# Optimization experiments

Measured on AMD Instinct MI355X. Metric: run time of the kernel, lower is better.

Reference implementation:

```python
import jax, jax.numpy as jnp
import numpy as np

B, T, C, H = 2, 2048, 1024, 16
HS = C // H  # head size = 64


def _rope_cos_sin(t, hs):
    # theta_i = 1/10000^(2(i-1)/hs) for i in [1, hs/2]
    pos = jnp.arange(t, dtype=jnp.float32)[:, None]          # [T,1]
    i = jnp.arange(1, hs // 2 + 1, dtype=jnp.float32)[None]  # [1,hs/2]
    theta = 1.0 / 10000.0 ** (2.0 * (i - 1.0) / hs)
    ang = pos * theta                                        # [T,hs/2]
    return jnp.cos(ang), jnp.sin(ang)


def _apply_rope(u, cos, sin):
    # u: [B,H,T,HS]; complex multiply on consecutive pairs
    u2 = u.reshape(*u.shape[:-1], HS // 2, 2)
    x0, x1 = u2[..., 0], u2[..., 1]
    c = cos[None, None]  # [1,1,T,hs/2]
    s = sin[None, None]
    r0 = x0 * c - x1 * s
    r1 = x0 * s + x1 * c
    return jnp.stack([r0, r1], axis=-1).reshape(u.shape)


def setup_inputs() -> dict:
    key = jax.random.key(0)
    ks = jax.random.split(key, 5)
    return {
        "x": jax.random.normal(ks[0], (B, T, C), dtype=jnp.float32),
        "W_qkv": jax.random.normal(ks[1], (C, 3 * C), dtype=jnp.float32) * 0.02,
        "b_qkv": jax.random.normal(ks[2], (3 * C,), dtype=jnp.float32) * 0.02,
        "W_proj": jax.random.normal(ks[3], (C, C), dtype=jnp.float32) * 0.02,
        "b_proj": jax.random.normal(ks[4], (C,), dtype=jnp.float32) * 0.02,
    }


def reference(x, W_qkv, b_qkv, W_proj, b_proj):
    b, t, c = x.shape
    qkv = x @ W_qkv + b_qkv                                   # [B,T,3C]
    qkv = qkv.reshape(b, t, H, 3 * HS).transpose(0, 2, 1, 3)  # [B,H,T,3*HS]
    q, k, v = jnp.split(qkv, 3, axis=-1)                      # each [B,H,T,HS]

    cos, sin = _rope_cos_sin(t, HS)
    q = _apply_rope(q, cos, sin)
    k = _apply_rope(k, cos, sin)

    att = jnp.einsum("bhqd,bhkd->bhqk", q, k) / jnp.sqrt(jnp.float32(HS))
    causal = jnp.tril(jnp.ones((t, t), dtype=bool))[None, None]
    att = jnp.where(causal, att, jnp.float32(-1e9))
    att = jax.nn.softmax(att, axis=-1)
    y = jnp.einsum("bhqk,bhkd->bhqd", att, v)                 # [B,H,T,HS]
    y = y.transpose(0, 2, 1, 3).reshape(b, t, c)
    return y @ W_proj + b_proj
```

## Files before the change

### kernel.cpp

```cpp
#include <hip/hip_runtime.h>

typedef unsigned short u16;
typedef unsigned int u32;
typedef __bf16 bf16x8 __attribute__((ext_vector_type(8)));
typedef float f32x4 __attribute__((ext_vector_type(4)));
typedef float f32x16 __attribute__((ext_vector_type(16)));
typedef u32 u32x4 __attribute__((ext_vector_type(4)));
typedef u16 u16x4 __attribute__((ext_vector_type(4)));
typedef u16 u16x8 __attribute__((ext_vector_type(8)));

__device__ __forceinline__ u16 f2bf(float f) {
  u32 u = __builtin_bit_cast(u32, f);
  u += 0x7fffu + ((u >> 16) & 1u);
  return (u16)(u >> 16);
}

__device__ __forceinline__ u32 pk2(float a, float b) {
  u32 ua = __builtin_bit_cast(u32, a) + 0x8000u;
  u32 ub = __builtin_bit_cast(u32, b) + 0x8000u;
  return __builtin_amdgcn_perm(ub, ua, 0x07060302);
}

__device__ __forceinline__ u32 cpk(float a, float b) {
  u32 r;
  asm("v_cvt_pk_bf16_f32 %0, %1, %2" : "=v"(r) : "v"(a), "v"(b));
  return r;
}

__device__ __forceinline__ void gld16(const void* g, void* l) {
  __builtin_amdgcn_global_load_lds(
      (const __attribute__((address_space(1))) void*)g,
      (__attribute__((address_space(3))) void*)l, 16, 0, 0);
}

__global__ __launch_bounds__(256) void k_prep(
    const float* __restrict__ x, u16* __restrict__ xb,
    const float* __restrict__ Wqkv, u16* __restrict__ Wqkvt,
    const float* __restrict__ Wproj, u16* __restrict__ Wpt,
    float2* __restrict__ rope) {
  __shared__ float tile[32][33];
  const int tid = threadIdx.x;
  int bx = blockIdx.x;
  if (bx < 4096) {
    int i = (bx * 256 + tid) * 4;
    float4 v = *(const float4*)(x + i);
    u16x4 o = { f2bf(v.x), f2bf(v.y), f2bf(v.z), f2bf(v.w) };
    *(u16x4*)(xb + i) = o;
    return;
  }
  bx -= 4096;
  const float* src; u16* dst; int R, Cc, bxx, byy;
  if (bx < 3072) {
    src = Wqkv; dst = Wqkvt; R = 1024; Cc = 3072; bxx = bx % 96; byy = bx / 96;
  } else if (bx < 4096) {
    int b = bx - 3072;
    src = Wproj; dst = Wpt; R = 1024; Cc = 1024; bxx = b % 32; byy = b / 32;
  } else {
    int i = (bx - 4096) * 256 + tid;
    int t = i >> 5, d = i & 31;
    float theta = expf(-(float)d * 0.28782313662425575f);
    float ang = (float)t * theta;
    rope[i] = make_float2(cosf(ang), sinf(ang));
    return;
  }
  int xx = tid & 31, yy = tid >> 5;
  int c0 = bxx * 32, r0 = byy * 32;
  for (int i = 0; i < 4; ++i)
    tile[yy + 8 * i][xx] = src[(size_t)(r0 + yy + 8 * i) * Cc + c0 + xx];
  __syncthreads();
  for (int i = 0; i < 4; ++i)
    dst[(size_t)(c0 + yy + 8 * i) * R + r0 + xx] = f2bf(tile[xx][yy + 8 * i]);
}

__global__ __launch_bounds__(256, 4) void k_qkv(
    const u16* __restrict__ Xb,
    const u16* __restrict__ Wt,
    const float* __restrict__ bias,
    const float2* __restrict__ rope,
    u16* __restrict__ Qg,
    u16* __restrict__ Kg,
    u16* __restrict__ Vt) {
  __shared__ alignas(16) u16 smem[18432];
  u16* As = smem;
  u16* Bs = smem + 8192;
  const int tid = threadIdx.x;
  const int lane = tid & 63, w = tid >> 6;
  const int quad = lane >> 4, l15 = lane & 15;
  const int m0 = blockIdx.y * 128, n0 = blockIdx.x * 128;
  const int wm = (w & 1) * 64, wn = (w >> 1) * 64;
  const int srow = lane >> 3, sj = lane & 7;
  const int sw = (sj ^ srow) * 8;
  const f32x4 vzero = {0.f, 0.f, 0.f, 0.f};

  f32x4 acc[4][4];
  for (int i = 0; i < 4; ++i)
    for (int j = 0; j < 4; ++j) acc[i][j] = vzero;

  for (int kt = 0; kt < 1024; kt += 64) {
    __syncthreads();
    for (int i = 0; i < 4; ++i) {
      int row = w * 32 + i * 8;
      gld16(Xb + (size_t)(m0 + row + srow) * 1024 + kt + sw, &As[row * 64]);
      gld16(Wt + (size_t)(n0 + row + srow) * 1024 + kt + sw, &Bs[row * 64]);
    }
    __syncthreads();
    for (int ks = 0; ks < 2; ++ks) {
      const int cc = ((ks * 4 + quad) ^ (l15 & 7)) * 8;
      bf16x8 a[4], b[4];
      for (int mt = 0; mt < 4; ++mt)
        a[mt] = *(const bf16x8*)&As[(wm + mt * 16 + l15) * 64 + cc];
      for (int nt = 0; nt < 4; ++nt)
        b[nt] = *(const bf16x8*)&Bs[(wn + nt * 16 + l15) * 64 + cc];
      for (int nt = 0; nt < 4; ++nt)
        for (int mt = 0; mt < 4; ++mt)
          acc[nt][mt] = __builtin_amdgcn_mfma_f32_16x16x32_bf16(
              b[nt], a[mt], acc[nt][mt], 0, 0, 0);
    }
  }
  __syncthreads();

  const int half = w >> 1;
  const int nh = n0 + half * 64;
  const int region = (nh % 192) >> 6;
  u16* Eh = smem + half * 9216;
  if (region < 2) {
    const float qsc = (region == 0) ? 0.18033688011112042f : 1.0f;
    for (int nt = 0; nt < 4; ++nt) {
      float4 bv4 = *(const float4*)&bias[nh + nt * 16 + quad * 4];
      for (int mt = 0; mt < 4; ++mt) {
        int m_l = wm + mt * 16 + l15;
        int t = (m0 + m_l) & 2047;
        float4 cs = *(const float4*)&rope[t * 32 + nt * 8 + quad * 2];
        float v0 = acc[nt][mt][0] + bv4.x;
        float v1 = acc[nt][mt][1] + bv4.y;
        float v2 = acc[nt][mt][2] + bv4.z;
        float v3 = acc[nt][mt][3] + bv4.w;
        float r0 = fmaf(-v1, cs.y, v0 * cs.x) * qsc;
        float r1 = fmaf( v0, cs.y, v1 * cs.x) * qsc;
        float r2 = fmaf(-v3, cs.w, v2 * cs.z) * qsc;
        float r3 = fmaf( v2, cs.w, v3 * cs.z) * qsc;
        uint2 pv; pv.x = pk2(r0, r1); pv.y = pk2(r2, r3);
        *(uint2*)&Eh[m_l * 72 + nt * 16 + quad * 4] = pv;
      }
    }
  } else {
    for (int nt = 0; nt < 4; ++nt) {
      float4 bv4 = *(const float4*)&bias[nh + nt * 16 + quad * 4];
      for (int mt = 0; mt < 4; ++mt) {
        int m_l = wm + mt * 16 + l15;
        int cb = nt * 16 + quad * 4;
        Eh[(cb + 0) * 136 + m_l] = f2bf(acc[nt][mt][0] + bv4.x);
        Eh[(cb + 1) * 136 + m_l] = f2bf(acc[nt][mt][1] + bv4.y);
        Eh[(cb + 2) * 136 + m_l] = f2bf(acc[nt][mt][2] + bv4.z);
        Eh[(cb + 3) * 136 + m_l] = f2bf(acc[nt][mt][3] + bv4.w);
      }
    }
  }
  __syncthreads();

  const int bb = m0 >> 11, t0 = m0 & 2047;
  for (int hf = 0; hf < 2; ++hf) {
    const int nhf = n0 + hf * 64;
    const int hh = nhf / 192;
    const int reg = (nhf % 192) >> 6;
    const u16* Ef = smem + hf * 9216;
    if (reg < 2) {
      u16* dst = (reg == 0 ? Qg : Kg) +
                 ((size_t)(bb * 16 + hh) * 2048 + t0) * 64;
      int chunk = tid & 7, row0 = tid >> 3;
      for (int p = 0; p < 4; ++p) {
        int row = row0 + p * 32;
        u16x8 val = *(const u16x8*)&Ef[row * 72 + chunk * 8];
        *(u16x8*)(dst + (size_t)row * 64 + chunk * 8) = val;
      }
    } else {
      u16* dstv = Vt + (size_t)(bb * 16 + hh) * 64 * 2048 + t0;
      int mch = tid & 15, c0r = tid >> 4;
      for (int p = 0; p < 4; ++p) {
        int c = c0r + p * 16;
        u16x8 val = *(const u16x8*)&Ef[c * 136 + mch * 8];
        *(u16x8*)(dstv + (size_t)c * 2048 + mch * 8) = val;
      }
    }
  }
}

__global__ __launch_bounds__(128, 2) void k_attn(
    const u16* __restrict__ Qg, const u16* __restrict__ Kg,
    const u16* __restrict__ Vt, u16* __restrict__ Og) {
  __shared__ alignas(16) u16 Ks[2][64 * 64];
  __shared__ alignas(16) u16 Vs[2][64 * 64];
  const int tid = threadIdx.x, lane = tid & 63, w = tid >> 6;
  const int q32 = lane & 31, hi = lane >> 5;
  const int id = blockIdx.x;
  const int xr = id & 7, p = id >> 3;
  const int g = p >> 5, pp = p & 31;
  const int t = (g & 1) ? pp : 31 - pp;
  const int bh = g * 8 + xr;
  const int nkb = t + 1;
  const u16* Qh = Qg + (size_t)bh * 2048 * 64;
  const u16* Kh = Kg + (size_t)bh * 2048 * 64;
  const u16* Vh = Vt + (size_t)bh * 64 * 2048;
  const int bb = bh >> 4, h = bh & 15;
  const int q0 = t * 64 + w * 32;

  const int r8 = lane >> 3, j8 = lane & 7;
  const int sw_c = (j8 ^ r8) * 8;

  auto stage = [&](int i, int b) {
    const int kk0 = i * 64;
    for (int tt = 0; tt < 4; ++tt) {
      int row = w * 32 + tt * 8;
      gld16(Kh + (size_t)(kk0 + row + r8) * 64 + sw_c, &Ks[b][row * 64]);
      gld16(Vh + (size_t)(row + r8) * 2048 + kk0 + sw_c, &Vs[b][row * 64]);
    }
  };

  bf16x8 aq[4];
  {
    const u16* qp = Qh + (size_t)(q0 + q32) * 64 + hi * 8;
#pragma unroll
    for (int ds = 0; ds < 4; ++ds) aq[ds] = *(const bf16x8*)(qp + ds * 16);
  }
  asm volatile("" ::: "memory");
  stage(0, 0);
  stage(1, 1);

  const u32x4 onesw = {0x3F803F80u, 0x3F803F80u, 0x3F803F80u, 0x3F803F80u};
  const bf16x8 ones = __builtin_bit_cast(bf16x8, onesw);

  f32x16 O0 = {}, O1 = {};
  f32x16 Lacc = {};

  for (int it = 0; it < nkb; ++it) {
    const int buf = it & 1;
    if (it == nkb - 1) asm volatile("s_waitcnt vmcnt(0)" ::: "memory");
    else               asm volatile("s_waitcnt vmcnt(8)" ::: "memory");
    asm volatile("s_barrier" ::: "memory");

    const int k0 = it * 64;
    f32x16 st0 = {}, st1 = {};
    __builtin_amdgcn_s_setprio(1);
#pragma unroll
    for (int ds = 0; ds < 4; ++ds) {
      const int c = ((ds * 2 + hi) ^ (q32 & 7)) * 8;
      bf16x8 ak0 = *(const bf16x8*)&Ks[buf][q32 * 64 + c];
      bf16x8 ak1 = *(const bf16x8*)&Ks[buf][(32 + q32) * 64 + c];
      st0 = __builtin_amdgcn_mfma_f32_32x32x16_bf16(ak0, aq[ds], st0, 0, 0, 0);
      st1 = __builtin_amdgcn_mfma_f32_32x32x16_bf16(ak1, aq[ds], st1, 0, 0, 0);
    }
    __builtin_amdgcn_s_setprio(0);

    float p0[16], p1[16];
    if (it == nkb - 1) {
      const int q = q0 + q32;
#pragma unroll
      for (int r = 0; r < 16; ++r) {
        int kk = k0 + (r & 3) + 8 * (r >> 2) + 4 * hi;
        float e0 = __builtin_amdgcn_exp2f(st0[r]);
        float e1 = __builtin_amdgcn_exp2f(st1[r]);
        p0[r] = (kk <= q) ? e0 : 0.f;
        p1[r] = (kk + 32 <= q) ? e1 : 0.f;
      }
    } else {
#pragma unroll
      for (int r = 0; r < 16; ++r) {
        p0[r] = __builtin_amdgcn_exp2f(st0[r]);
        p1[r] = __builtin_amdgcn_exp2f(st1[r]);
      }
    }

    u32 paw[4][4];
#pragma unroll
    for (int kt = 0; kt < 2; ++kt) {
      const float* P = kt ? p1 : p0;
#pragma unroll
      for (int kl = 0; kl < 2; ++kl) {
        const int b0i = kl * 8;
        u32 a0 = cpk(P[b0i + 0], P[b0i + 1]);
        u32 b0 = cpk(P[b0i + 4], P[b0i + 5]);
        u32 a1 = cpk(P[b0i + 2], P[b0i + 3]);
        u32 b1 = cpk(P[b0i + 6], P[b0i + 7]);
        asm volatile("v_permlane32_swap_b32 %0, %1" : "+v"(a0), "+v"(b0));
        asm volatile("v_permlane32_swap_b32 %0, %1" : "+v"(a1), "+v"(b1));
        const int s = kt * 2 + kl;
        paw[s][0] = a0; paw[s][1] = a1; paw[s][2] = b0; paw[s][3] = b1;
      }
    }

    __builtin_amdgcn_s_setprio(1);
#pragma unroll
    for (int s = 0; s < 4; ++s) {
      u32x4 pw = { paw[s][0], paw[s][1], paw[s][2], paw[s][3] };
      bf16x8 pa = __builtin_bit_cast(bf16x8, pw);
      const int c = ((s * 2 + hi) ^ (q32 & 7)) * 8;
      bf16x8 bv0 = *(const bf16x8*)&Vs[buf][q32 * 64 + c];
      bf16x8 bv1 = *(const bf16x8*)&Vs[buf][(32 + q32) * 64 + c];
      O0 = __builtin_amdgcn_mfma_f32_32x32x16_bf16(pa, bv0, O0, 0, 0, 0);
      O1 = __builtin_amdgcn_mfma_f32_32x32x16_bf16(pa, bv1, O1, 0, 0, 0);
      Lacc = __builtin_amdgcn_mfma_f32_32x32x16_bf16(pa, ones, Lacc, 0, 0, 0);
    }
    __builtin_amdgcn_s_setprio(0);

    asm volatile("s_barrier" ::: "memory");
    if (it + 2 < nkb) stage(it + 2, buf);
  }

  {
    u16* dst = Og + ((size_t)bb * 2048 + q0) * 1024 + h * 64 + q32;
#pragma unroll
    for (int r = 0; r < 16; ++r) {
      int qp = (r & 3) + 8 * (r >> 2) + 4 * hi;
      float iv = __builtin_amdgcn_rcpf(Lacc[r]);
      dst[(size_t)qp * 1024]      = f2bf(O0[r] * iv);
      dst[(size_t)qp * 1024 + 32] = f2bf(O1[r] * iv);
    }
  }
}

__global__ __launch_bounds__(256, 4) void k_proj(
    const u16* __restrict__ Ag,
    const u16* __restrict__ Wt,
    const float* __restrict__ bias,
    float* __restrict__ out) {
  __shared__ alignas(16) u16 As[64 * 64];
  __shared__ alignas(16) u16 Bs[128 * 64];
  const int tid = threadIdx.x;
  const int lane = tid & 63, w = tid >> 6;
  const int quad = lane >> 4, l15 = lane & 15;
  const int m0 = blockIdx.y * 64, n0 = blockIdx.x * 128;
  const int wm = (w & 1) * 32, wn = (w >> 1) * 64;
  const int srow = lane >> 3, sj = lane & 7;
  const int sw = (sj ^ srow) * 8;
  const f32x4 vzero = {0.f, 0.f, 0.f, 0.f};

  f32x4 acc[2][4];
  for (int i = 0; i < 2; ++i)
    for (int j = 0; j < 4; ++j) acc[i][j] = vzero;

  for (int kt = 0; kt < 1024; kt += 64) {
    __syncthreads();
    for (int i = 0; i < 2; ++i) {
      int row = w * 16 + i * 8;
      gld16(Ag + (size_t)(m0 + row + srow) * 1024 + kt + sw, &As[row * 64]);
    }
    for (int i = 0; i < 4; ++i) {
      int row = w * 32 + i * 8;
      gld16(Wt + (size_t)(n0 + row + srow) * 1024 + kt + sw, &Bs[row * 64]);
    }
    __syncthreads();
    for (int ks = 0; ks < 2; ++ks) {
      const int cc = ((ks * 4 + quad) ^ (l15 & 7)) * 8;
      bf16x8 a[2], b[4];
      for (int mt = 0; mt < 2; ++mt)
        a[mt] = *(const bf16x8*)&As[(wm + mt * 16 + l15) * 64 + cc];
      for (int nt = 0; nt < 4; ++nt)
        b[nt] = *(const bf16x8*)&Bs[(wn + nt * 16 + l15) * 64 + cc];
      for (int mt = 0; mt < 2; ++mt)
        for (int nt = 0; nt < 4; ++nt)
          acc[mt][nt] = __builtin_amdgcn_mfma_f32_16x16x32_bf16(
              a[mt], b[nt], acc[mt][nt], 0, 0, 0);
    }
  }

  for (int nt = 0; nt < 4; ++nt) {
    int n = n0 + wn + nt * 16 + l15;
    float bv = bias[n];
    for (int mt = 0; mt < 2; ++mt)
      for (int r = 0; r < 4; ++r) {
        int m = m0 + wm + mt * 16 + quad * 4 + r;
        out[(size_t)m * 1024 + n] = acc[mt][nt][r] + bv;
      }
  }
}

extern "C" void kernel_launch(void* const* d_in, const int* in_sizes, int n_in,
                              void* d_out, int out_size, void* d_ws, size_t ws_size,
                              hipStream_t stream) {
  (void)in_sizes; (void)n_in; (void)out_size; (void)ws_size;
  const float* x     = (const float*)d_in[0];
  const float* Wqkv  = (const float*)d_in[1];
  const float* bqkv  = (const float*)d_in[2];
  const float* Wproj = (const float*)d_in[3];
  const float* bproj = (const float*)d_in[4];
  float* out = (float*)d_out;

  char* ws = (char*)d_ws;
  size_t off = 0;
  u16* Xb    = (u16*)(ws + off); off += (size_t)4096 * 1024 * 2;
  u16* Wqkvt = (u16*)(ws + off); off += (size_t)3072 * 1024 * 2;
  u16* Wpt   = (u16*)(ws + off); off += (size_t)1024 * 1024 * 2;
  u16* Qg    = (u16*)(ws + off); off += (size_t)2 * 16 * 2048 * 64 * 2;
  u16* Kg    = (u16*)(ws + off); off += (size_t)2 * 16 * 2048 * 64 * 2;
  u16* Vt    = (u16*)(ws + off); off += (size_t)2 * 16 * 64 * 2048 * 2;
  u16* Att   = (u16*)(ws + off); off += (size_t)4096 * 1024 * 2;
  float2* rope = (float2*)(ws + off); off += (size_t)2048 * 32 * sizeof(float2);

  k_prep<<<8448, 256, 0, stream>>>(x, Xb, Wqkv, Wqkvt, Wproj, Wpt, rope);
  k_qkv<<<dim3(24, 32), 256, 0, stream>>>(Xb, Wqkvt, bqkv, rope, Qg, Kg, Vt);
  k_attn<<<1024, 128, 0, stream>>>(Qg, Kg, Vt, Att);
  k_proj<<<dim3(8, 64), 256, 0, stream>>>(Att, Wpt, bproj, out);
}
```

Baseline: 170.2 us.

## Split attention KV range in two halves and merge partials in new kernel

Each query tile's causal key range is split into two halves processed by separate blocks (2048 blocks instead of 1024), which writes unnormalized fp32 partial outputs and row sums. A new merge kernel adds the halves, normalizes, and writes bf16 output. The aim is better load balance and occupancy for long causal rows, at the cost of an extra launch and about 32MB of fp32 partial traffic. Merging without a max rescale is valid because the softmax has no max subtraction (exp2 of raw scores).

```diff
diff --git a/kernel.cpp b/kernel.cpp
--- a/kernel.cpp
+++ b/kernel.cpp
@@ -187,30 +187,35 @@
 
 __global__ __launch_bounds__(128, 2) void k_attn(
     const u16* __restrict__ Qg, const u16* __restrict__ Kg,
-    const u16* __restrict__ Vt, u16* __restrict__ Og) {
+    const u16* __restrict__ Vt, float* __restrict__ PartO,
+    float* __restrict__ PartL) {
   __shared__ alignas(16) u16 Ks[2][64 * 64];
   __shared__ alignas(16) u16 Vs[2][64 * 64];
   const int tid = threadIdx.x, lane = tid & 63, w = tid >> 6;
   const int q32 = lane & 31, hi = lane >> 5;
   const int id = blockIdx.x;
-  const int xr = id & 7, p = id >> 3;
-  const int g = p >> 5, pp = p & 31;
-  const int t = (g & 1) ? pp : 31 - pp;
+  const int xr = id & 7, rest = id >> 3;
+  const int g = rest >> 6;
+  int u = rest & 63;
+  if (g & 1) u = 63 - u;
+  const int tt = u >> 1, hf = u & 1;
   const int bh = g * 8 + xr;
-  const int nkb = t + 1;
+  const int nk = tt + 1;
+  const int c = (nk + 1) >> 1;
+  const int lo = hf ? c : 0, hiE = hf ? nk : c;
+  const int n = hiE - lo;
   const u16* Qh = Qg + (size_t)bh * 2048 * 64;
   const u16* Kh = Kg + (size_t)bh * 2048 * 64;
   const u16* Vh = Vt + (size_t)bh * 64 * 2048;
-  const int bb = bh >> 4, h = bh & 15;
-  const int q0 = t * 64 + w * 32;
+  const int q0 = tt * 64 + w * 32;
 
   const int r8 = lane >> 3, j8 = lane & 7;
   const int sw_c = (j8 ^ r8) * 8;
 
-  auto stage = [&](int i, int b) {
-    const int kk0 = i * 64;
-    for (int tt = 0; tt < 4; ++tt) {
-      int row = w * 32 + tt * 8;
+  auto stage = [&](int kb, int b) {
+    const int kk0 = kb * 64;
+    for (int tt2 = 0; tt2 < 4; ++tt2) {
+      int row = w * 32 + tt2 * 8;
       gld16(Kh + (size_t)(kk0 + row + r8) * 64 + sw_c, &Ks[b][row * 64]);
       gld16(Vh + (size_t)(row + r8) * 2048 + kk0 + sw_c, &Vs[b][row * 64]);
     }
@@ -223,8 +228,9 @@
     for (int ds = 0; ds < 4; ++ds) aq[ds] = *(const bf16x8*)(qp + ds * 16);
   }
   asm volatile("" ::: "memory");
-  stage(0, 0);
-  stage(1, 1);
+
+  if (n > 0) stage(lo, 0);
+  if (n > 1) stage(lo + 1, 1);
 
   const u32x4 onesw = {0x3F803F80u, 0x3F803F80u, 0x3F803F80u, 0x3F803F80u};
   const bf16x8 ones = __builtin_bit_cast(bf16x8, onesw);
@@ -232,27 +238,28 @@
   f32x16 O0 = {}, O1 = {};
   f32x16 Lacc = {};
 
-  for (int it = 0; it < nkb; ++it) {
-    const int buf = it & 1;
-    if (it == nkb - 1) asm volatile("s_waitcnt vmcnt(0)" ::: "memory");
-    else               asm volatile("s_waitcnt vmcnt(8)" ::: "memory");
+  for (int i = 0; i < n; ++i) {
+    const int kb = lo + i;
+    const int buf = i & 1;
+    if (i == n - 1) asm volatile("s_waitcnt vmcnt(0)" ::: "memory");
+    else            asm volatile("s_waitcnt vmcnt(8)" ::: "memory");
     asm volatile("s_barrier" ::: "memory");
 
-    const int k0 = it * 64;
+    const int k0 = kb * 64;
     f32x16 st0 = {}, st1 = {};
     __builtin_amdgcn_s_setprio(1);
 #pragma unroll
     for (int ds = 0; ds < 4; ++ds) {
-      const int c = ((ds * 2 + hi) ^ (q32 & 7)) * 8;
-      bf16x8 ak0 = *(const bf16x8*)&Ks[buf][q32 * 64 + c];
-      bf16x8 ak1 = *(const bf16x8*)&Ks[buf][(32 + q32) * 64 + c];
+      const int cc = ((ds * 2 + hi) ^ (q32 & 7)) * 8;
+      bf16x8 ak0 = *(const bf16x8*)&Ks[buf][q32 * 64 + cc];
+      bf16x8 ak1 = *(const bf16x8*)&Ks[buf][(32 + q32) * 64 + cc];
       st0 = __builtin_amdgcn_mfma_f32_32x32x16_bf16(ak0, aq[ds], st0, 0, 0, 0);
       st1 = __builtin_amdgcn_mfma_f32_32x32x16_bf16(ak1, aq[ds], st1, 0, 0, 0);
     }
     __builtin_amdgcn_s_setprio(0);
 
     float p0[16], p1[16];
-    if (it == nkb - 1) {
+    if (kb == nk - 1) {
       const int q = q0 + q32;
 #pragma unroll
       for (int r = 0; r < 16; ++r) {
@@ -293,9 +300,9 @@
     for (int s = 0; s < 4; ++s) {
       u32x4 pw = { paw[s][0], paw[s][1], paw[s][2], paw[s][3] };
       bf16x8 pa = __builtin_bit_cast(bf16x8, pw);
-      const int c = ((s * 2 + hi) ^ (q32 & 7)) * 8;
-      bf16x8 bv0 = *(const bf16x8*)&Vs[buf][q32 * 64 + c];
-      bf16x8 bv1 = *(const bf16x8*)&Vs[buf][(32 + q32) * 64 + c];
+      const int cc = ((s * 2 + hi) ^ (q32 & 7)) * 8;
+      bf16x8 bv0 = *(const bf16x8*)&Vs[buf][q32 * 64 + cc];
+      bf16x8 bv1 = *(const bf16x8*)&Vs[buf][(32 + q32) * 64 + cc];
       O0 = __builtin_amdgcn_mfma_f32_32x32x16_bf16(pa, bv0, O0, 0, 0, 0);
       O1 = __builtin_amdgcn_mfma_f32_32x32x16_bf16(pa, bv1, O1, 0, 0, 0);
       Lacc = __builtin_amdgcn_mfma_f32_32x32x16_bf16(pa, ones, Lacc, 0, 0, 0);
@@ -303,18 +310,48 @@
     __builtin_amdgcn_s_setprio(0);
 
     asm volatile("s_barrier" ::: "memory");
-    if (it + 2 < nkb) stage(it + 2, buf);
+    if (i + 2 < n) stage(lo + i + 2, buf);
   }
 
   {
-    u16* dst = Og + ((size_t)bb * 2048 + q0) * 1024 + h * 64 + q32;
+    const int pid = ((bh * 32 + tt) * 2 + hf);
+    float* po = PartO + (size_t)pid * 4096 + (size_t)(w * 32) * 64;
+    float* pl = PartL + (size_t)pid * 64 + w * 32;
 #pragma unroll
     for (int r = 0; r < 16; ++r) {
       int qp = (r & 3) + 8 * (r >> 2) + 4 * hi;
-      float iv = __builtin_amdgcn_rcpf(Lacc[r]);
-      dst[(size_t)qp * 1024]      = f2bf(O0[r] * iv);
-      dst[(size_t)qp * 1024 + 32] = f2bf(O1[r] * iv);
-    }
+      po[qp * 64 + q32]      = O0[r];
+      po[qp * 64 + 32 + q32] = O1[r];
+      if (q32 == 0) pl[qp] = Lacc[r];
+    }
+  }
+}
+
+__global__ __launch_bounds__(128) void k_fmerge(
+    const float* __restrict__ PartO, const float* __restrict__ PartL,
+    u16* __restrict__ Og) {
+  const int tg = blockIdx.x;
+  const int bh = tg >> 5, tt = tg & 31;
+  const int bb = bh >> 4, h = bh & 15;
+  const int tid = threadIdx.x;
+  const int r = tid >> 1, seg = tid & 1;
+  const float* pa = PartO + (size_t)(tg * 2 + 0) * 4096 + r * 64 + seg * 32;
+  const float* pb = PartO + (size_t)(tg * 2 + 1) * 4096 + r * 64 + seg * 32;
+  const float la = PartL[(size_t)(tg * 2 + 0) * 64 + r];
+  const float lb = PartL[(size_t)(tg * 2 + 1) * 64 + r];
+  const float iv = 1.0f / (la + lb);
+  u16* dst = Og + ((size_t)(bb * 2048 + tt * 64 + r)) * 1024 + h * 64 + seg * 32;
+#pragma unroll
+  for (int c8 = 0; c8 < 4; ++c8) {
+    float4 a0 = *(const float4*)(pa + c8 * 8);
+    float4 a1 = *(const float4*)(pa + c8 * 8 + 4);
+    float4 b0 = *(const float4*)(pb + c8 * 8);
+    float4 b1 = *(const float4*)(pb + c8 * 8 + 4);
+    u16x8 o = { f2bf((a0.x + b0.x) * iv), f2bf((a0.y + b0.y) * iv),
+                f2bf((a0.z + b0.z) * iv), f2bf((a0.w + b0.w) * iv),
+                f2bf((a1.x + b1.x) * iv), f2bf((a1.y + b1.y) * iv),
+                f2bf((a1.z + b1.z) * iv), f2bf((a1.w + b1.w) * iv) };
+    *(u16x8*)(dst + c8 * 8) = o;
   }
 }
 
@@ -395,9 +432,12 @@
   u16* Vt    = (u16*)(ws + off); off += (size_t)2 * 16 * 64 * 2048 * 2;
   u16* Att   = (u16*)(ws + off); off += (size_t)4096 * 1024 * 2;
   float2* rope = (float2*)(ws + off); off += (size_t)2048 * 32 * sizeof(float2);
+  float* PartO = (float*)(ws + off); off += (size_t)2048 * 4096 * 4;
+  float* PartL = (float*)(ws + off); off += (size_t)2048 * 64 * 4;
 
   k_prep<<<8448, 256, 0, stream>>>(x, Xb, Wqkv, Wqkvt, Wproj, Wpt, rope);
   k_qkv<<<dim3(24, 32), 256, 0, stream>>>(Xb, Wqkvt, bqkv, rope, Qg, Kg, Vt);
-  k_attn<<<1024, 128, 0, stream>>>(Qg, Kg, Vt, Att);
+  k_attn<<<2048, 128, 0, stream>>>(Qg, Kg, Vt, PartO, PartL);
+  k_fmerge<<<1024, 128, 0, stream>>>(PartO, PartL, Att);
   k_proj<<<dim3(8, 64), 256, 0, stream>>>(Att, Wpt, bproj, out);
 }
```

Result: slower. 180.2 us (+5.9%).
